# Kernel optimization log

Hardware: AMD Instinct MI355X
Metric: run time of the kernel (lower is better)

## Reference

```python
import jax, jax.numpy as jnp
import numpy as np

NEG_SLOPE = 0.2   # PyG GATConv default negative_slope
BN_EPS = 1e-5


def gat_conv(x, W, att_src, att_dst, bias, src, dst, num_nodes, concat):
    """PyG-style GATConv (eval mode, no dropout). att_*: [H, C]."""
    H, C = att_src.shape
    h = (x @ W).reshape(-1, H, C)                       # [N, H, C]
    a_src = jnp.sum(h * att_src[None], axis=-1)         # [N, H]
    a_dst = jnp.sum(h * att_dst[None], axis=-1)         # [N, H]
    e = jax.nn.leaky_relu(a_src[src] + a_dst[dst], NEG_SLOPE)  # [E, H]
    # segment softmax over incoming edges of each dst node
    m = jax.ops.segment_max(e, dst, num_segments=num_nodes)
    m = jnp.where(jnp.isfinite(m), m, 0.0)
    p = jnp.exp(e - m[dst])
    s = jax.ops.segment_sum(p, dst, num_segments=num_nodes)
    alpha = p / (s[dst] + 1e-16)                        # [E, H]
    msg = h[src] * alpha[:, :, None]                    # [E, H, C]
    out = jax.ops.segment_sum(msg, dst, num_segments=num_nodes)  # [N, H, C]
    out = out.reshape(num_nodes, H * C) if concat else out.mean(axis=1)
    return out + bias


def bn_eval(x, gamma, beta, mean, var):
    return (x - mean) * jax.lax.rsqrt(var + BN_EPS) * gamma + beta


def setup_inputs() -> dict:
    N, E = 50000, 800000
    IN, HID, HEADS, OUT = 22, 64, 4, 32
    key = jax.random.key(0)
    ks = jax.random.split(key, 12)
    d = {}
    d["x"] = jax.random.normal(ks[0], (N, IN), dtype=jnp.float32)
    d["edge_index"] = jax.random.randint(ks[1], (2, E), 0, N, dtype=jnp.int64)
    d["W1"] = jax.random.normal(ks[2], (IN, HEADS * HID), dtype=jnp.float32) * 0.2
    d["att_src1"] = jax.random.normal(ks[3], (HEADS, HID), dtype=jnp.float32) * 0.1
    d["att_dst1"] = jax.random.normal(ks[4], (HEADS, HID), dtype=jnp.float32) * 0.1
    d["b1"] = jnp.zeros((HEADS * HID,), dtype=jnp.float32)
    # GAT layer 2: 256 -> 32, 1 head, no concat (mean)
    d["W2"] = jax.random.normal(ks[5], (HEADS * HID, OUT), dtype=jnp.float32) * 0.06
    d["att_src2"] = jax.random.normal(ks[6], (1, OUT), dtype=jnp.float32) * 0.1
    d["att_dst2"] = jax.random.normal(ks[7], (1, OUT), dtype=jnp.float32) * 0.1
    d["b2"] = jnp.zeros((OUT,), dtype=jnp.float32)
    # BatchNorm params (eval mode)
    d["gamma1"] = jnp.ones((HEADS * HID,), dtype=jnp.float32)
    d["beta1"] = jnp.zeros((HEADS * HID,), dtype=jnp.float32)
    d["mean1"] = jax.random.normal(ks[8], (HEADS * HID,), dtype=jnp.float32) * 0.05
    d["var1"] = jnp.ones((HEADS * HID,), dtype=jnp.float32)
    d["gamma2"] = jnp.ones((OUT,), dtype=jnp.float32)
    d["beta2"] = jnp.zeros((OUT,), dtype=jnp.float32)
    d["mean2"] = jax.random.normal(ks[9], (OUT,), dtype=jnp.float32) * 0.05
    d["var2"] = jnp.ones((OUT,), dtype=jnp.float32)
    return d


def reference(x, edge_index, W1, att_src1, att_dst1, b1, W2, att_src2, att_dst2, b2,
              gamma1, beta1, mean1, var1, gamma2, beta2, mean2, var2):
    N = x.shape[0]
    # PyG GATConv adds self-loops by default
    loops = jnp.arange(N, dtype=edge_index.dtype)
    src = jnp.concatenate([edge_index[0], loops])
    dst = jnp.concatenate([edge_index[1], loops])
    h = gat_conv(x, W1, att_src1, att_dst1, b1, src, dst, N, concat=True)
    h = jax.nn.elu(bn_eval(h, gamma1, beta1, mean1, var1))
    # dropout: identity in eval mode
    h = gat_conv(h, W2, att_src2, att_dst2, b2, src, dst, N, concat=False)
    h = jax.nn.elu(bn_eval(h, gamma2, beta2, mean2, var2))
    return h
```

## Files before the change

### kernel.cpp

```cpp
#include <hip/hip_runtime.h>
#include <hip/hip_fp16.h>
#include <math.h>

#define NN   50000
#define EE   800000
#define ETOT 850000
#define INF_FEATS 22
#define D1   256
#define NH   4
#define D2   32
#define BN_EPS 1e-5f
#define NEG_SLOPE 0.2f
#define SCAN_B 49
#define CNT_BLOCKS ((ETOT + 255) / 256)

typedef _Float16 f16x8 __attribute__((ext_vector_type(8)));
typedef float f32x4 __attribute__((ext_vector_type(4)));

__device__ __forceinline__ float wsum64(float v) {
#pragma unroll
    for (int m = 32; m > 0; m >>= 1) v += __shfl_xor(v, m);
    return v;
}

__device__ __forceinline__ float2 h2f(unsigned u) {
    __half2 h = *reinterpret_cast<__half2*>(&u);
    return __half22float2(h);
}

__global__ __launch_bounds__(256) void sAB_count(
    const float* __restrict__ x, const float* __restrict__ W1,
    const float* __restrict__ atts, const float* __restrict__ attd,
    const int* __restrict__ ei, __half* __restrict__ h1h,
    float* __restrict__ as1, float* __restrict__ ad1, int* __restrict__ cnt) {
    if (blockIdx.x >= NN) {
        const int e = (blockIdx.x - NN) * 256 + threadIdx.x;
        if (e < ETOT) {
            int dst = (e < EE) ? ei[EE + e] : (e - EE);
            atomicAdd(&cnt[dst], 1);
        }
        return;
    }
    const int n = blockIdx.x, col = threadIdx.x;
    float a = 0.f;
#pragma unroll
    for (int k = 0; k < INF_FEATS; ++k)
        a = fmaf(x[n * INF_FEATS + k], W1[k * D1 + col], a);
    h1h[n * D1 + col] = __float2half(a);
    const int w = col >> 6, lane = col & 63;
    const float s = wsum64(a * atts[col]);
    const float d = wsum64(a * attd[col]);
    if (lane == 0) {
        as1[n * NH + w] = s;
        ad1[n * NH + w] = d;
    }
}

__global__ __launch_bounds__(1024) void scan_a(const int* __restrict__ cnt,
                                               int* __restrict__ offs,
                                               int* __restrict__ bsum) {
    __shared__ int sh[1024];
    const int t = threadIdx.x, i = blockIdx.x * 1024 + t;
    const int v = (i < NN) ? cnt[i] : 0;
    sh[t] = v;
    __syncthreads();
    for (int off = 1; off < 1024; off <<= 1) {
        int u = (t >= off) ? sh[t - off] : 0;
        __syncthreads();
        sh[t] += u;
        __syncthreads();
    }
    if (i < NN) offs[i] = sh[t] - v;
    if (t == 1023) bsum[blockIdx.x] = sh[1023];
}

__global__ __launch_bounds__(1024) void scan_c(int* __restrict__ offs,
                                               const int* __restrict__ bsum,
                                               int* __restrict__ cur) {
    __shared__ int sbase;
    if (threadIdx.x == 0) {
        int r = 0;
        for (int b = 0; b < blockIdx.x; ++b) r += bsum[b];
        sbase = r;
    }
    __syncthreads();
    const int i = blockIdx.x * 1024 + threadIdx.x;
    if (i < NN) {
        const int o = offs[i] + sbase;
        offs[i] = o;
        cur[i] = o;
    }
    if (i == 0) offs[NN] = ETOT;
}

__global__ void c_scatter(const int* __restrict__ ei, int* __restrict__ cur,
                          int* __restrict__ ssrc) {
    int e = blockIdx.x * blockDim.x + threadIdx.x;
    if (e >= ETOT) return;
    int src, dst;
    if (e < EE) { src = ei[e]; dst = ei[EE + e]; }
    else        { src = dst = e - EE; }
    int pos = atomicAdd(&cur[dst], 1);
    ssrc[pos] = src;
}

__global__ __launch_bounds__(256) void g1k(
    const uint2* __restrict__ h1q, const float* __restrict__ as1,
    const float* __restrict__ ad1, const int* __restrict__ offs,
    const int* __restrict__ ssrc, const float* __restrict__ b1,
    const float* __restrict__ g1, const float* __restrict__ be1,
    const float* __restrict__ mu1, const float* __restrict__ va1,
    uint2* __restrict__ hposth) {
    const int wv = threadIdx.x >> 6, lane = threadIdx.x & 63;
    const int n = blockIdx.x * 4 + wv;
    const int off = offs[n];
    const int deg = offs[n + 1] - off;
    const int h = lane >> 4;
    const float adst = ad1[n * NH + h];
    float a0 = 0.f, a1 = 0.f, a2 = 0.f, a3 = 0.f, ssum = 0.f;
    for (int p = 0; p < deg; p += 8) {
        int sj[8];
        float al[8];
#pragma unroll
        for (int u = 0; u < 8; ++u)
            sj[u] = (p + u < deg) ? ssrc[off + p + u] : ssrc[off];
#pragma unroll
        for (int u = 0; u < 8; ++u) {
            float a = as1[sj[u] * NH + h] + adst;
            a = (a >= 0.f) ? a : NEG_SLOPE * a;
            al[u] = (p + u < deg) ? __expf(a) : 0.f;
        }
        uint2 hv[8];
#pragma unroll
        for (int u = 0; u < 8; ++u)
            hv[u] = h1q[(size_t)sj[u] * 64 + lane];
#pragma unroll
        for (int u = 0; u < 8; ++u) {
            ssum += al[u];
            const float2 f0 = h2f(hv[u].x), f1 = h2f(hv[u].y);
            a0 = fmaf(al[u], f0.x, a0);
            a1 = fmaf(al[u], f0.y, a1);
            a2 = fmaf(al[u], f1.x, a2);
            a3 = fmaf(al[u], f1.y, a3);
        }
    }
    const float inv = 1.f / (ssum + 1e-16f);
    const float4 bb = ((const float4*)b1)[lane];
    const float4 mm = ((const float4*)mu1)[lane];
    const float4 vv = ((const float4*)va1)[lane];
    const float4 gg = ((const float4*)g1)[lane];
    const float4 ee = ((const float4*)be1)[lane];
    float4 o;
    o.x = (a0 * inv + bb.x - mm.x) * rsqrtf(vv.x + BN_EPS) * gg.x + ee.x;
    o.y = (a1 * inv + bb.y - mm.y) * rsqrtf(vv.y + BN_EPS) * gg.y + ee.y;
    o.z = (a2 * inv + bb.z - mm.z) * rsqrtf(vv.z + BN_EPS) * gg.z + ee.z;
    o.w = (a3 * inv + bb.w - mm.w) * rsqrtf(vv.w + BN_EPS) * gg.w + ee.w;
    o.x = (o.x > 0.f) ? o.x : expm1f(o.x);
    o.y = (o.y > 0.f) ? o.y : expm1f(o.y);
    o.z = (o.z > 0.f) ? o.z : expm1f(o.z);
    o.w = (o.w > 0.f) ? o.w : expm1f(o.w);
    __half2 p01 = __floats2half2_rn(o.x, o.y);
    __half2 p23 = __floats2half2_rn(o.z, o.w);
    uint2 st;
    st.x = *reinterpret_cast<unsigned*>(&p01);
    st.y = *reinterpret_cast<unsigned*>(&p23);
    hposth[(size_t)n * 64 + lane] = st;
}

__global__ __launch_bounds__(256) void sFGm(
    const uint4* __restrict__ hq,
    const float* __restrict__ W2,
    const float* __restrict__ atts, const float* __restrict__ attd,
    __half* __restrict__ h2h, float* __restrict__ as2, float* __restrict__ ad2) {
    const int w = threadIdx.x >> 6, l = threadIdx.x & 63;
    const int row0 = blockIdx.x * 64 + w * 16;
    const int lmod = l & 15, ldiv = l >> 4;
    f16x8 b0[8], b1[8];
#pragma unroll
    for (int ks = 0; ks < 8; ++ks) {
#pragma unroll
        for (int j = 0; j < 8; ++j) {
            const int k = ks * 32 + ldiv * 8 + j;
            b0[ks][j] = (_Float16)W2[k * D2 + lmod];
            b1[ks][j] = (_Float16)W2[k * D2 + lmod + 16];
        }
    }
    f32x4 acc0 = {0.f, 0.f, 0.f, 0.f}, acc1 = {0.f, 0.f, 0.f, 0.f};
    const int arow = min(row0 + lmod, NN - 1);
    const uint4* ap = hq + (size_t)arow * 32 + ldiv;
#pragma unroll
    for (int ks = 0; ks < 8; ++ks) {
        uint4 av = ap[ks * 4];
        f16x8 a = *reinterpret_cast<f16x8*>(&av);
        acc0 = __builtin_amdgcn_mfma_f32_16x16x32_f16(a, b0[ks], acc0, 0, 0, 0);
        acc1 = __builtin_amdgcn_mfma_f32_16x16x32_f16(a, b1[ks], acc1, 0, 0, 0);
    }
    const float a2s0 = atts[lmod], a2s1 = atts[lmod + 16];
    const float a2d0 = attd[lmod], a2d1 = attd[lmod + 16];
#pragma unroll
    for (int i = 0; i < 4; ++i) {
        const int r = row0 + ldiv * 4 + i;
        const bool ok = r < NN;
        if (ok) {
            h2h[(size_t)r * D2 + lmod]      = __float2half(acc0[i]);
            h2h[(size_t)r * D2 + lmod + 16] = __float2half(acc1[i]);
        }
        float s = acc0[i] * a2s0 + acc1[i] * a2s1;
        float d = acc0[i] * a2d0 + acc1[i] * a2d1;
#pragma unroll
        for (int m = 8; m > 0; m >>= 1) {
            s += __shfl_xor(s, m);
            d += __shfl_xor(d, m);
        }
        if (ok && lmod == 0) { as2[r] = s; ad2[r] = d; }
    }
}

__global__ __launch_bounds__(256) void g2k(
    const unsigned short* __restrict__ h2u, const float* __restrict__ as2,
    const float* __restrict__ ad2, const int* __restrict__ offs,
    const int* __restrict__ ssrc, const float* __restrict__ b2,
    const float* __restrict__ g2, const float* __restrict__ be2,
    const float* __restrict__ mu2, const float* __restrict__ va2,
    float* __restrict__ out) {
    const int t = threadIdx.x;
    const int n = blockIdx.x * 8 + (t >> 5), c = t & 31;
    const int off = offs[n];
    const int deg = offs[n + 1] - off;
    const float adst = ad2[n];
    float ssum = 0.f, acc = 0.f;
    for (int p = 0; p < deg; p += 8) {
        int sj[8];
        float al[8];
#pragma unroll
        for (int u = 0; u < 8; ++u)
            sj[u] = (p + u < deg) ? ssrc[off + p + u] : ssrc[off];
#pragma unroll
        for (int u = 0; u < 8; ++u) {
            float a = as2[sj[u]] + adst;
            a = (a >= 0.f) ? a : NEG_SLOPE * a;
            al[u] = (p + u < deg) ? __expf(a) : 0.f;
        }
        unsigned short hv[8];
#pragma unroll
        for (int u = 0; u < 8; ++u)
            hv[u] = h2u[sj[u] * D2 + c];
#pragma unroll
        for (int u = 0; u < 8; ++u) {
            ssum += al[u];
            acc = fmaf(al[u], __half2float(*reinterpret_cast<__half*>(&hv[u])), acc);
        }
    }
    float v = acc / (ssum + 1e-16f) + b2[c];
    v = (v - mu2[c]) * rsqrtf(va2[c] + BN_EPS) * g2[c] + be2[c];
    v = (v > 0.f) ? v : expm1f(v);
    out[n * D2 + c] = v;
}

extern "C" void kernel_launch(void* const* d_in, const int* in_sizes, int n_in,
                              void* d_out, int out_size, void* d_ws, size_t ws_size,
                              hipStream_t stream) {
    (void)in_sizes; (void)n_in; (void)out_size; (void)ws_size;
    const float* x    = (const float*)d_in[0];
    const int*   ei   = (const int*)  d_in[1];
    const float* W1   = (const float*)d_in[2];
    const float* as1i = (const float*)d_in[3];
    const float* ad1i = (const float*)d_in[4];
    const float* b1   = (const float*)d_in[5];
    const float* W2   = (const float*)d_in[6];
    const float* as2i = (const float*)d_in[7];
    const float* ad2i = (const float*)d_in[8];
    const float* b2   = (const float*)d_in[9];
    const float* g1   = (const float*)d_in[10];
    const float* be1  = (const float*)d_in[11];
    const float* mu1  = (const float*)d_in[12];
    const float* va1  = (const float*)d_in[13];
    const float* g2   = (const float*)d_in[14];
    const float* be2  = (const float*)d_in[15];
    const float* mu2  = (const float*)d_in[16];
    const float* va2  = (const float*)d_in[17];
    float* out = (float*)d_out;

    float* ws = (float*)d_ws;
    __half* hposth = (__half*)ws;
    float* as1  = ws + (size_t)NN * (D1 / 2);
    float* ad1  = as1 + (size_t)NN * NH;
    float* as2  = ad1 + (size_t)NN * NH;
    float* ad2  = as2 + NN;
    __half* h1h = (__half*)(ad2 + NN);
    __half* h2h = h1h + (size_t)NN * D1;
    int* cnt   = (int*)(h2h + (size_t)NN * D2);
    int* offs  = cnt + NN;
    int* cur   = offs + NN + 1;
    int* ssrc  = cur + NN;
    int* bsum  = ssrc + ETOT;

    hipMemsetAsync(cnt, 0, NN * sizeof(int), stream);

    sAB_count<<<NN + CNT_BLOCKS, 256, 0, stream>>>(x, W1, as1i, ad1i, ei,
                                                   h1h, as1, ad1, cnt);
    scan_a<<<SCAN_B, 1024, 0, stream>>>(cnt, offs, bsum);
    scan_c<<<SCAN_B, 1024, 0, stream>>>(offs, bsum, cur);
    c_scatter<<<(ETOT + 255) / 256, 256, 0, stream>>>(ei, cur, ssrc);
    g1k<<<NN / 4, 256, 0, stream>>>((const uint2*)h1h, as1, ad1, offs, ssrc,
                                    b1, g1, be1, mu1, va1, (uint2*)hposth);
    sFGm<<<(NN + 63) / 64, 256, 0, stream>>>((const uint4*)hposth, W2,
                                             as2i, ad2i, h2h, as2, ad2);
    g2k<<<NN / 8, 256, 0, stream>>>((const unsigned short*)h2h, as2, ad2, offs,
                                    ssrc, b2, g2, be2, mu2, va2, out);
}
```

Before: 347.7 us.

## Reuse count-phase atomic ranks for CSR scatter and batch 8 rows per projection block

During degree counting, each edge now saves the value returned by its atomicAdd as a rank. The scatter kernel then writes ssrc at offs[dst]+rank[e] without a second atomic pass, and the per-node cursor array is removed. Separately, the layer-1 projection processes 8 nodes per block, staging their x rows in shared memory and loading each W1 column once per block instead of once per node. The cost is an extra rank array (written once, read once) and more registers per thread in the projection.

```diff
diff --git a/kernel.cpp b/kernel.cpp
--- a/kernel.cpp
+++ b/kernel.cpp
@@ -12,6 +12,8 @@
 #define BN_EPS 1e-5f
 #define NEG_SLOPE 0.2f
 #define SCAN_B 49
+#define AB_ROWS 8
+#define AB_BLOCKS (NN / AB_ROWS)
 #define CNT_BLOCKS ((ETOT + 255) / 256)
 
 typedef _Float16 f16x8 __attribute__((ext_vector_type(8)));
@@ -32,27 +34,43 @@
     const float* __restrict__ x, const float* __restrict__ W1,
     const float* __restrict__ atts, const float* __restrict__ attd,
     const int* __restrict__ ei, __half* __restrict__ h1h,
-    float* __restrict__ as1, float* __restrict__ ad1, int* __restrict__ cnt) {
-    if (blockIdx.x >= NN) {
-        const int e = (blockIdx.x - NN) * 256 + threadIdx.x;
+    float* __restrict__ as1, float* __restrict__ ad1,
+    int* __restrict__ cnt, int* __restrict__ rank) {
+    if (blockIdx.x >= AB_BLOCKS) {
+        const int e = (blockIdx.x - AB_BLOCKS) * 256 + threadIdx.x;
         if (e < ETOT) {
             int dst = (e < EE) ? ei[EE + e] : (e - EE);
-            atomicAdd(&cnt[dst], 1);
+            rank[e] = atomicAdd(&cnt[dst], 1);
         }
         return;
     }
-    const int n = blockIdx.x, col = threadIdx.x;
-    float a = 0.f;
-#pragma unroll
-    for (int k = 0; k < INF_FEATS; ++k)
-        a = fmaf(x[n * INF_FEATS + k], W1[k * D1 + col], a);
-    h1h[n * D1 + col] = __float2half(a);
-    const int w = col >> 6, lane = col & 63;
-    const float s = wsum64(a * atts[col]);
-    const float d = wsum64(a * attd[col]);
-    if (lane == 0) {
-        as1[n * NH + w] = s;
-        ad1[n * NH + w] = d;
+    __shared__ float xs[AB_ROWS][INF_FEATS];
+    const int t = threadIdx.x;
+    const int n0 = blockIdx.x * AB_ROWS;
+    for (int i = t; i < AB_ROWS * INF_FEATS; i += 256)
+        xs[i / INF_FEATS][i % INF_FEATS] = x[n0 * INF_FEATS + i];
+    __syncthreads();
+    float acc[AB_ROWS];
+#pragma unroll
+    for (int r = 0; r < AB_ROWS; ++r) acc[r] = 0.f;
+#pragma unroll
+    for (int k = 0; k < INF_FEATS; ++k) {
+        const float wv = W1[k * D1 + t];
+#pragma unroll
+        for (int r = 0; r < AB_ROWS; ++r) acc[r] = fmaf(xs[r][k], wv, acc[r]);
+    }
+    const float asv = atts[t], adv = attd[t];
+    const int w = t >> 6, lane = t & 63;
+#pragma unroll
+    for (int r = 0; r < AB_ROWS; ++r) {
+        const int n = n0 + r;
+        h1h[(size_t)n * D1 + t] = __float2half(acc[r]);
+        const float s = wsum64(acc[r] * asv);
+        const float d = wsum64(acc[r] * adv);
+        if (lane == 0) {
+            as1[n * NH + w] = s;
+            ad1[n * NH + w] = d;
+        }
     }
 }
 
@@ -75,8 +93,7 @@
 }
 
 __global__ __launch_bounds__(1024) void scan_c(int* __restrict__ offs,
-                                               const int* __restrict__ bsum,
-                                               int* __restrict__ cur) {
+                                               const int* __restrict__ bsum) {
     __shared__ int sbase;
     if (threadIdx.x == 0) {
         int r = 0;
@@ -85,23 +102,20 @@
     }
     __syncthreads();
     const int i = blockIdx.x * 1024 + threadIdx.x;
-    if (i < NN) {
-        const int o = offs[i] + sbase;
-        offs[i] = o;
-        cur[i] = o;
-    }
+    if (i < NN) offs[i] += sbase;
     if (i == 0) offs[NN] = ETOT;
 }
 
-__global__ void c_scatter(const int* __restrict__ ei, int* __restrict__ cur,
-                          int* __restrict__ ssrc) {
+__global__ void c_scatter2(const int* __restrict__ ei,
+                           const int* __restrict__ offs,
+                           const int* __restrict__ rank,
+                           int* __restrict__ ssrc) {
     int e = blockIdx.x * blockDim.x + threadIdx.x;
     if (e >= ETOT) return;
     int src, dst;
     if (e < EE) { src = ei[e]; dst = ei[EE + e]; }
     else        { src = dst = e - EE; }
-    int pos = atomicAdd(&cur[dst], 1);
-    ssrc[pos] = src;
+    ssrc[offs[dst] + rank[e]] = src;
 }
 
 __global__ __launch_bounds__(256) void g1k(
@@ -291,17 +305,17 @@
     __half* h2h = h1h + (size_t)NN * D1;
     int* cnt   = (int*)(h2h + (size_t)NN * D2);
     int* offs  = cnt + NN;
-    int* cur   = offs + NN + 1;
-    int* ssrc  = cur + NN;
+    int* rank  = offs + NN + 1;
+    int* ssrc  = rank + ETOT;
     int* bsum  = ssrc + ETOT;
 
     hipMemsetAsync(cnt, 0, NN * sizeof(int), stream);
 
-    sAB_count<<<NN + CNT_BLOCKS, 256, 0, stream>>>(x, W1, as1i, ad1i, ei,
-                                                   h1h, as1, ad1, cnt);
+    sAB_count<<<AB_BLOCKS + CNT_BLOCKS, 256, 0, stream>>>(
+        x, W1, as1i, ad1i, ei, h1h, as1, ad1, cnt, rank);
     scan_a<<<SCAN_B, 1024, 0, stream>>>(cnt, offs, bsum);
-    scan_c<<<SCAN_B, 1024, 0, stream>>>(offs, bsum, cur);
-    c_scatter<<<(ETOT + 255) / 256, 256, 0, stream>>>(ei, cur, ssrc);
+    scan_c<<<SCAN_B, 1024, 0, stream>>>(offs, bsum);
+    c_scatter2<<<(ETOT + 255) / 256, 256, 0, stream>>>(ei, offs, rank, ssrc);
     g1k<<<NN / 4, 256, 0, stream>>>((const uint2*)h1h, as1, ad1, offs, ssrc,
                                     b1, g1, be1, mu1, va1, (uint2*)hposth);
     sFGm<<<(NN + 63) / 64, 256, 0, stream>>>((const uint4*)hposth, W2,
```

New measurement: 315.9 us. -9.1%, faster.
